# Performance work log

Measured on AMD Instinct MI355X. Metric: run time of the kernel, lower is better.

## Reference

```python
import jax, jax.numpy as jnp
import numpy as np

B, P, ENC = 64, 196, 512
EMB = ATT = DEC = 256
V = 10000
T = 44


def setup_inputs() -> dict:
    key = jax.random.key(0)
    ks = jax.random.split(key, 16)
    def xavier(k, shape):
        fan_out, fan_in = shape
        std = (2.0 / (fan_in + fan_out)) ** 0.5
        return jax.random.normal(k, shape, dtype=jnp.float32) * std
    return {
        "encoder_out": jax.random.normal(ks[0], (B, P, ENC), dtype=jnp.float32),
        "caption": jax.random.randint(ks[1], (B, T), 0, V),
        "W_enc_att": xavier(ks[2], (ATT, ENC)),
        "W_dec_att": xavier(ks[3], (ATT, DEC)),
        "W_full": xavier(ks[4], (1, ATT)),
        "embedding": jax.random.normal(ks[5], (V, EMB), dtype=jnp.float32) * 0.02,
        "W_init_h": xavier(ks[6], (DEC, ENC)),
        "b_init_h": jnp.zeros((DEC,), dtype=jnp.float32),
        "W_init_c": xavier(ks[7], (DEC, ENC)),
        "b_init_c": jnp.zeros((DEC,), dtype=jnp.float32),
        "W_ih": jax.random.normal(ks[8], (4 * DEC, EMB + ENC), dtype=jnp.float32) * 0.03,
        "b_ih": jnp.zeros((4 * DEC,), dtype=jnp.float32),
        "W_hh": jax.random.normal(ks[9], (4 * DEC, DEC), dtype=jnp.float32) * 0.03,
        "b_hh": jnp.zeros((4 * DEC,), dtype=jnp.float32),
        "W_out": xavier(ks[10], (V, DEC)),
        "b_out": jnp.zeros((V,), dtype=jnp.float32),
    }


def _decoder(encoder_out, caption, W_enc_att, W_dec_att, W_full, embedding,
             W_init_h, b_init_h, W_init_c, b_init_c,
             W_ih, b_ih, W_hh, b_hh, W_out, b_out):
    # embeddings: [B, T, EMB] -> time-major [T, B, EMB]
    emb = embedding[caption].transpose(1, 0, 2)
    # init hidden state from mean pooled encoder features
    avg = encoder_out.mean(axis=1)                      # [B, ENC]
    h0 = avg @ W_init_h.T + b_init_h                    # [B, DEC]
    c0 = avg @ W_init_c.T + b_init_c
    # attention key projection of encoder, constant over time
    att1 = jnp.einsum('bpe,ae->bpa', encoder_out, W_enc_att)  # [B, P, ATT]

    def step(carry, emb_t):
        h, c = carry
        # additive attention
        att2 = h @ W_dec_att.T                          # [B, ATT]
        scores = jnp.einsum('bpa,a->bp',
                            jax.nn.relu(att1 + att2[:, None, :]), W_full[0])
        alpha = jax.nn.softmax(scores, axis=1)          # [B, P]
        ctx = jnp.einsum('bp,bpe->be', alpha, encoder_out)  # [B, ENC]
        # LSTM cell (torch gate order: i, f, g, o)
        x = jnp.concatenate([ctx, emb_t], axis=1)       # [B, ENC+EMB]
        gates = x @ W_ih.T + b_ih + h @ W_hh.T + b_hh   # [B, 4*DEC]
        i, f, g, o = jnp.split(gates, 4, axis=1)
        c_new = jax.nn.sigmoid(f) * c + jax.nn.sigmoid(i) * jnp.tanh(g)
        h_new = jax.nn.sigmoid(o) * jnp.tanh(c_new)
        logits = h_new @ W_out.T + b_out                # [B, V]
        return (h_new, c_new), (logits, alpha)

    # NOTE: torch cat order is [weighted_context, embedding]
    (_, _), (logits, alphas) = jax.lax.scan(step, (h0, c0), emb)
    predictions = logits.transpose(1, 0, 2)             # [B, T, V]
    alphas = alphas.transpose(1, 0, 2)                  # [B, T, P]
    return predictions, alphas


def reference(encoder_out, caption, W_enc_att, W_dec_att, W_full, embedding,
              W_init_h, b_init_h, W_init_c, b_init_c,
              W_ih, b_ih, W_hh, b_hh, W_out, b_out):
    return _decoder(encoder_out, caption, W_enc_att, W_dec_att, W_full, embedding,
                    W_init_h, b_init_h, W_init_c, b_init_c,
                    W_ih, b_ih, W_hh, b_hh, W_out, b_out)
```

## Files before the change

kernel.cpp:

```cpp
#include <hip/hip_runtime.h>

#define B_   64
#define P_   196
#define ENC_ 512
#define ATT_ 256
#define DEC_ 256
#define EMB_ 256
#define V_   10000
#define T_   44
#define G4_  1024
#define XW_  768
#define A1N_ 26624

using short8 = __attribute__((ext_vector_type(8))) short;
using half8  = __attribute__((ext_vector_type(8))) _Float16;
using f32x4  = __attribute__((ext_vector_type(4))) float;
typedef _Float16 f16x2 __attribute__((ext_vector_type(2)));

__device__ __forceinline__ unsigned short f2bf(float f) {
    unsigned int u = __float_as_uint(f);
    unsigned int r = (u + 0x7fffu + ((u >> 16) & 1u)) >> 16;
    return (unsigned short)r;
}

__device__ __forceinline__ unsigned int pkh2(float a, float b) {
    f16x2 t; t.x = (_Float16)a; t.y = (_Float16)b;
    return __builtin_bit_cast(unsigned int, t);
}

__device__ __forceinline__ float fdot2f(float wbits, f16x2 xv, float acc) {
    f16x2 wv = __builtin_bit_cast(f16x2, wbits);
#if __has_builtin(__builtin_amdgcn_fdot2)
    return __builtin_amdgcn_fdot2(wv, xv, acc, false);
#else
    acc = fmaf((float)wv.x, (float)xv.x, acc);
    acc = fmaf((float)wv.y, (float)xv.y, acc);
    return acc;
#endif
}
__device__ __forceinline__ float fdot2u(unsigned int wbits, f16x2 xv, float acc) {
    f16x2 wv = __builtin_bit_cast(f16x2, wbits);
#if __has_builtin(__builtin_amdgcn_fdot2)
    return __builtin_amdgcn_fdot2(wv, xv, acc, false);
#else
    acc = fmaf((float)wv.x, (float)xv.x, acc);
    acc = fmaf((float)wv.y, (float)xv.y, acc);
    return acc;
#endif
}

__device__ __forceinline__ void bar() {
    asm volatile("s_waitcnt lgkmcnt(0)" ::: "memory");
    __builtin_amdgcn_s_barrier();
    asm volatile("" ::: "memory");
}

__global__ void k_transpose(const float* __restrict__ src, float* __restrict__ dst,
                            int N, int stride, int off) {
    __shared__ float t[32][33];
    int k0 = blockIdx.x * 32, n0 = blockIdx.y * 32;
    int tx = threadIdx.x & 31, ty = threadIdx.x >> 5;
    for (int r = ty; r < 32; r += 8)
        t[r][tx] = src[(size_t)(n0 + r) * stride + off + k0 + tx];
    __syncthreads();
    for (int r = ty; r < 32; r += 8)
        dst[(size_t)(k0 + r) * N + n0 + tx] = t[tx][r];
}

__global__ __launch_bounds__(256) void k_packWda(const float* __restrict__ Wda,
                                                 float4* __restrict__ WdaP4) {
    int d4 = blockIdx.x, a = threadIdx.x;
    float4 v;
    v.x = Wda[(size_t)a * DEC_ + 4 * d4 + 0];
    v.y = Wda[(size_t)a * DEC_ + 4 * d4 + 1];
    v.z = Wda[(size_t)a * DEC_ + 4 * d4 + 2];
    v.w = Wda[(size_t)a * DEC_ + 4 * d4 + 3];
    WdaP4[(size_t)d4 * 256 + a] = v;
}

__global__ __launch_bounds__(256) void k_packWg(const float* __restrict__ Wih,
        const float* __restrict__ Whh, float4* __restrict__ Wg4) {
    int k2 = blockIdx.x, d = threadIdx.x;
    int k = 2 * k2;
    unsigned int o[4];
#pragma unroll
    for (int g = 0; g < 4; ++g) {
        int row = g * 256 + d;
        float a0, a1;
        if (k < ENC_) {
            a0 = Wih[(size_t)row * XW_ + k];
            a1 = Wih[(size_t)row * XW_ + k + 1];
        } else {
            a0 = Whh[(size_t)row * DEC_ + k - ENC_];
            a1 = Whh[(size_t)row * DEC_ + k - ENC_ + 1];
        }
        o[g] = pkh2(a0, a1);
    }
    float4 v;
    v.x = __builtin_bit_cast(float, o[0]);
    v.y = __builtin_bit_cast(float, o[1]);
    v.z = __builtin_bit_cast(float, o[2]);
    v.w = __builtin_bit_cast(float, o[3]);
    Wg4[(size_t)k2 * 256 + d] = v;
}

__global__ __launch_bounds__(256) void k_packenc(const float* __restrict__ enc,
                                                 uint2* __restrict__ encPh) {
    int b = blockIdx.x, p4b = blockIdx.y * 7;
    for (int p4 = p4b; p4 < p4b + 7; ++p4) {
        for (int e = threadIdx.x; e < ENC_; e += 256) {
            float a0 = enc[((size_t)b * P_ + 4 * p4 + 0) * ENC_ + e];
            float a1 = enc[((size_t)b * P_ + 4 * p4 + 1) * ENC_ + e];
            float a2 = enc[((size_t)b * P_ + 4 * p4 + 2) * ENC_ + e];
            float a3 = enc[((size_t)b * P_ + 4 * p4 + 3) * ENC_ + e];
            uint2 v; v.x = pkh2(a0, a1); v.y = pkh2(a2, a3);
            encPh[((size_t)b * 49 + p4) * ENC_ + e] = v;
        }
    }
}

__global__ void k_cvt(const float* __restrict__ src, unsigned short* __restrict__ dst, int n) {
    int i = blockIdx.x * 256 + threadIdx.x;
    if (i < n) dst[i] = f2bf(src[i]);
}

__global__ __launch_bounds__(256) void k_init_state(
        const float* __restrict__ enc,
        const float* __restrict__ W_init_h, const float* __restrict__ b_init_h,
        const float* __restrict__ W_init_c, const float* __restrict__ b_init_c,
        float* __restrict__ h0, float* __restrict__ c0) {
    int b = blockIdx.x, tid = threadIdx.x;
    __shared__ float avg[ENC_];
    for (int e = tid; e < ENC_; e += 256) {
        float s = 0.f;
        const float* p = enc + (size_t)b * P_ * ENC_ + e;
        for (int i = 0; i < P_; i++) s += p[(size_t)i * ENC_];
        avg[e] = s * (1.0f / (float)P_);
    }
    __syncthreads();
    int d = tid;
    float hs = b_init_h[d], cs = b_init_c[d];
    const float* wh = W_init_h + (size_t)d * ENC_;
    const float* wc = W_init_c + (size_t)d * ENC_;
    for (int e = 0; e < ENC_; e++) { float a = avg[e]; hs += a * wh[e]; cs += a * wc[e]; }
    h0[b * DEC_ + d] = hs;
    c0[b * DEC_ + d] = cs;
}

__global__ __launch_bounds__(256) void k_att1(
        const float* __restrict__ enc, const float* __restrict__ Wea,
        unsigned int* __restrict__ att1h) {
    int n0 = blockIdx.x * 128;
    int m0 = blockIdx.y * 128;
    int b  = blockIdx.z;
    __shared__ __align__(16) unsigned short At[128][40];
    __shared__ __align__(16) unsigned short Bt[128][40];
    int tid = threadIdx.x;
    int lane = tid & 63, w = tid >> 6;
    int wm = (w & 1) * 64, wn = (w >> 1) * 64;
    f32x4 acc[4][4];
#pragma unroll
    for (int i = 0; i < 4; i++)
#pragma unroll
        for (int j = 0; j < 4; j++) acc[i][j] = (f32x4){0.f, 0.f, 0.f, 0.f};

    for (int k0 = 0; k0 < ENC_; k0 += 32) {
#pragma unroll
        for (int l = 0; l < 2; l++) {
            int idx = l * 256 + tid;
            int r = idx >> 2, kc = (idx & 3) * 8;
            const float* ap = Wea + (size_t)(m0 + r) * ENC_ + k0 + kc;
            float4 f0 = *reinterpret_cast<const float4*>(ap);
            float4 f1 = *reinterpret_cast<const float4*>(ap + 4);
            uint4 av;
            av.x = pkh2(f0.x, f0.y); av.y = pkh2(f0.z, f0.w);
            av.z = pkh2(f1.x, f1.y); av.w = pkh2(f1.z, f1.w);
            *reinterpret_cast<uint4*>(&At[r][kc]) = av;
            uint4 bv = make_uint4(0u, 0u, 0u, 0u);
            int p = n0 + r;
            if (p < P_) {
                const float* bp = enc + ((size_t)b * P_ + p) * ENC_ + k0 + kc;
                float4 g0 = *reinterpret_cast<const float4*>(bp);
                float4 g1 = *reinterpret_cast<const float4*>(bp + 4);
                bv.x = pkh2(g0.x, g0.y); bv.y = pkh2(g0.z, g0.w);
                bv.z = pkh2(g1.x, g1.y); bv.w = pkh2(g1.z, g1.w);
            }
            *reinterpret_cast<uint4*>(&Bt[r][kc]) = bv;
        }
        __syncthreads();
        int qk = (lane >> 4) * 8, fr = lane & 15;
        half8 a[4], bb[4];
#pragma unroll
        for (int i = 0; i < 4; i++) {
            a[i]  = *reinterpret_cast<const half8*>(&At[wm + i * 16 + fr][qk]);
            bb[i] = *reinterpret_cast<const half8*>(&Bt[wn + i * 16 + fr][qk]);
        }
#pragma unroll
        for (int i = 0; i < 4; i++)
#pragma unroll
            for (int j = 0; j < 4; j++)
                acc[i][j] = __builtin_amdgcn_mfma_f32_16x16x32_f16(a[i], bb[j], acc[i][j], 0, 0, 0);
        __syncthreads();
    }
    unsigned int* eb = att1h + (size_t)b * A1N_;
    int col = lane & 15, qr = (lane >> 4) * 4;
#pragma unroll
    for (int j = 0; j < 4; j++) {
        int p = n0 + wn + j * 16 + col;
        if (p < 208) {
#pragma unroll
            for (int i = 0; i < 4; i++) {
                int a0r = m0 + wm + i * 16 + qr;
                eb[(size_t)(a0r >> 1) * 208 + p]       = pkh2(acc[i][j][0], acc[i][j][1]);
                eb[(size_t)((a0r >> 1) + 1) * 208 + p] = pkh2(acc[i][j][2], acc[i][j][3]);
            }
        }
    }
}

__global__ __launch_bounds__(256) void k_embW(
        const int* __restrict__ caption, const float* __restrict__ embedding,
        const float* __restrict__ WiheT, const float* __restrict__ b_ih,
        const float* __restrict__ b_hh, float* __restrict__ embW) {
    int r0 = blockIdx.x * 16, tid = threadIdx.x;
    __shared__ float embL[16][256];
    __shared__ int capL[16];
    if (tid < 16) {
        int r = r0 + tid, t = r >> 6, b = r & 63;
        capL[tid] = caption[b * T_ + t];
    }
    __syncthreads();
#pragma unroll
    for (int lr = 0; lr < 16; lr++)
        embL[lr][tid] = embedding[(size_t)capL[lr] * EMB_ + tid];
    __syncthreads();
    float base0 = b_ih[tid] + b_hh[tid];
    float base1 = b_ih[tid + 256] + b_hh[tid + 256];
    float base2 = b_ih[tid + 512] + b_hh[tid + 512];
    float base3 = b_ih[tid + 768] + b_hh[tid + 768];
    float acc[16][4];
#pragma unroll
    for (int lr = 0; lr < 16; lr++) {
        acc[lr][0] = base0; acc[lr][1] = base1; acc[lr][2] = base2; acc[lr][3] = base3;
    }
    for (int e = 0; e < EMB_; e++) {
        const float* wr = WiheT + (size_t)e * G4_ + tid;
        float w0 = wr[0], w1 = wr[256], w2 = wr[512], w3 = wr[768];
#pragma unroll
        for (int lr = 0; lr < 16; lr++) {
            float ev = embL[lr][e];
            acc[lr][0] += w0 * ev; acc[lr][1] += w1 * ev;
            acc[lr][2] += w2 * ev; acc[lr][3] += w3 * ev;
        }
    }
#pragma unroll
    for (int lr = 0; lr < 16; lr++) {
        float* o = embW + (size_t)(r0 + lr) * G4_ + tid;
        o[0] = acc[lr][0]; o[256] = acc[lr][1]; o[512] = acc[lr][2]; o[768] = acc[lr][3];
    }
}

__global__ __launch_bounds__(1024, 4) void k_recur(
        const unsigned int* __restrict__ att1h, const float4* __restrict__ WdaP4,
        const float* __restrict__ W_full, const float4* __restrict__ Wg4,
        const float* __restrict__ embW, const uint2* __restrict__ encPh,
        const float* __restrict__ h0, const float* __restrict__ c0,
        unsigned short* __restrict__ Hbf, float* __restrict__ out_alpha) {
    int b = blockIdx.x, tid = threadIdx.x;
    int q = tid >> 8;
    int r = tid & 255;
    int e5 = tid & 511, ph = tid >> 9;

    __shared__ __align__(16) float h_l[DEC_];
    __shared__ __align__(16) float att2_l[ATT_];
    __shared__ __align__(16) float wf_l[ATT_];
    __shared__ __align__(16) _Float16 xh[XW_];
    __shared__ __align__(8)  _Float16 alpha_h[208];
    __shared__ float p1[4][256];
    __shared__ float p2[4][256];
    __shared__ float p3[2][512];
    __shared__ __align__(16) float4 p4s[4][256];
    __shared__ unsigned int att1_lds[A1N_ + 48];

    {
        const unsigned int* a1g = att1h + (size_t)b * A1N_;
        for (int i = tid; i < A1N_; i += 1024) att1_lds[i] = a1g[i];
    }
    if (tid < 256) {
        float hv = h0[b * DEC_ + tid];
        h_l[tid] = hv;
        xh[512 + tid] = (_Float16)hv;
        wf_l[tid] = W_full[tid];
    }
    float c = (tid < 256) ? c0[b * DEC_ + tid] : 0.f;
    __syncthreads();

    const uint2* encb = encPh + (size_t)b * (49 * ENC_);

    for (int t = 0; t < T_; ++t) {
        float a2 = 0.f;
#pragma unroll 4
        for (int i = 0; i < 16; i++) {
            int d4 = q * 16 + i;
            float4 w = WdaP4[(size_t)d4 * 256 + r];
            float4 h4 = *reinterpret_cast<const float4*>(&h_l[4 * d4]);
            a2 += w.x * h4.x + w.y * h4.y + w.z * h4.z + w.w * h4.w;
        }
        p1[q][r] = a2;
        bar();
        if (tid < 256) att2_l[tid] = p1[0][tid] + p1[1][tid] + p1[2][tid] + p1[3][tid];
        bar();

        float sp = 0.f;
#pragma unroll 4
        for (int i = 0; i < 32; i++) {
            int a2i = q * 32 + i;
            f16x2 av = __builtin_bit_cast(f16x2, att1_lds[a2i * 208 + r]);
            float2 t2 = *reinterpret_cast<const float2*>(&att2_l[2 * a2i]);
            float2 w4 = *reinterpret_cast<const float2*>(&wf_l[2 * a2i]);
            sp += fmaxf((float)av.x + t2.x, 0.f) * w4.x +
                  fmaxf((float)av.y + t2.y, 0.f) * w4.y;
        }
        p2[q][r] = sp;
        bar();

        float sden = 0.f;
        {
            int l = tid & 63;
#pragma unroll
            for (int cq = 0; cq < 4; cq++) {
                int cc = l + cq * 64;
                float s = p2[0][cc] + p2[1][cc] + p2[2][cc] + p2[3][cc];
                sden += (cc < P_) ? __expf(s) : 0.f;
            }
#pragma unroll
            for (int off = 32; off; off >>= 1) sden += __shfl_xor(sden, off);
        }
        if (tid < 256) {
            float s = p2[0][tid] + p2[1][tid] + p2[2][tid] + p2[3][tid];
            float ex = (tid < P_) ? __expf(s) : 0.f;
            float alpha = ex / sden;
            if (tid < 208) alpha_h[tid] = (_Float16)alpha;
            if (tid < P_) out_alpha[(size_t)b * (T_ * P_) + t * P_ + tid] = alpha;
        }
        bar();

        float cx = 0.f;
        {
            int p4b = ph ? 25 : 0, p4e = ph ? 49 : 25;
#pragma unroll 5
            for (int p4 = p4b; p4 < p4e; p4++) {
                uint2 ev = encb[(size_t)p4 * ENC_ + e5];
                f16x2 a01 = *reinterpret_cast<const f16x2*>(&alpha_h[4 * p4]);
                f16x2 a23 = *reinterpret_cast<const f16x2*>(&alpha_h[4 * p4 + 2]);
                cx = fdot2u(ev.x, a01, cx);
                cx = fdot2u(ev.y, a23, cx);
            }
        }
        p3[ph][e5] = cx;
        float ew0 = 0.f, ew1 = 0.f, ew2 = 0.f, ew3 = 0.f;
        if (tid < 256) {
            const float* ew = embW + ((size_t)t * B_ + b) * G4_;
            ew0 = ew[tid]; ew1 = ew[tid + 256]; ew2 = ew[tid + 512]; ew3 = ew[tid + 768];
        }
        bar();
        if (tid < 512) xh[tid] = (_Float16)(p3[0][tid] + p3[1][tid]);
        bar();

        float4 acc = {0.f, 0.f, 0.f, 0.f};
#pragma unroll 8
        for (int i = 0; i < 96; i++) {
            int k2 = q * 96 + i;
            float4 w = Wg4[(size_t)k2 * 256 + r];
            f16x2 xv = *reinterpret_cast<const f16x2*>(&xh[2 * k2]);
            acc.x = fdot2f(w.x, xv, acc.x);
            acc.y = fdot2f(w.y, xv, acc.y);
            acc.z = fdot2f(w.z, xv, acc.z);
            acc.w = fdot2f(w.w, xv, acc.w);
        }
        p4s[q][r] = acc;
        bar();

        if (tid < 256) {
            float4 g0 = p4s[0][tid], g1 = p4s[1][tid], g2 = p4s[2][tid], g3 = p4s[3][tid];
            float gi = g0.x + g1.x + g2.x + g3.x + ew0;
            float gf = g0.y + g1.y + g2.y + g3.y + ew1;
            float gg = g0.z + g1.z + g2.z + g3.z + ew2;
            float go = g0.w + g1.w + g2.w + g3.w + ew3;
            float i_g = 1.f / (1.f + __expf(-gi));
            float f_g = 1.f / (1.f + __expf(-gf));
            float g_g = tanhf(gg);
            float o_g = 1.f / (1.f + __expf(-go));
            c = f_g * c + i_g * g_g;
            float hn = o_g * tanhf(c);
            h_l[tid] = hn;
            xh[512 + tid] = (_Float16)hn;
            Hbf[((size_t)t * B_ + b) * DEC_ + tid] = f2bf(hn);
        }
        bar();
    }
}

__global__ __launch_bounds__(256) void k_logits(
        const unsigned short* __restrict__ Hbf, const unsigned short* __restrict__ Woutbf,
        const float* __restrict__ b_out, float* __restrict__ out) {
    int n0 = blockIdx.x * 128, m0 = blockIdx.y * 128;
    __shared__ __align__(16) unsigned short At[128][40];
    __shared__ __align__(16) unsigned short Bt[128][40];
    int tid = threadIdx.x;
    int lane = tid & 63, w = tid >> 6;
    int wm = (w & 1) * 64, wn = (w >> 1) * 64;
    f32x4 acc[4][4];
#pragma unroll
    for (int i = 0; i < 4; i++)
#pragma unroll
        for (int j = 0; j < 4; j++) acc[i][j] = (f32x4){0.f, 0.f, 0.f, 0.f};

    for (int k0 = 0; k0 < DEC_; k0 += 32) {
#pragma unroll
        for (int l = 0; l < 2; l++) {
            int idx = l * 256 + tid;
            int r = idx >> 2, kc = (idx & 3) * 8;
            uint4 av = *reinterpret_cast<const uint4*>(&Hbf[(size_t)(m0 + r) * DEC_ + k0 + kc]);
            *reinterpret_cast<uint4*>(&At[r][kc]) = av;
            uint4 bv = make_uint4(0u, 0u, 0u, 0u);
            if (n0 + r < V_)
                bv = *reinterpret_cast<const uint4*>(&Woutbf[(size_t)(n0 + r) * DEC_ + k0 + kc]);
            *reinterpret_cast<uint4*>(&Bt[r][kc]) = bv;
        }
        __syncthreads();
        int qk = (lane >> 4) * 8, fr = lane & 15;
        short8 a[4], bb[4];
#pragma unroll
        for (int i = 0; i < 4; i++) {
            a[i]  = *reinterpret_cast<const short8*>(&At[wm + i * 16 + fr][qk]);
            bb[i] = *reinterpret_cast<const short8*>(&Bt[wn + i * 16 + fr][qk]);
        }
#pragma unroll
        for (int i = 0; i < 4; i++)
#pragma unroll
            for (int j = 0; j < 4; j++)
                acc[i][j] = __builtin_amdgcn_mfma_f32_16x16x32_bf16(a[i], bb[j], acc[i][j], 0, 0, 0);
        __syncthreads();
    }
    int col = lane & 15, qr = (lane >> 4) * 4;
#pragma unroll
    for (int j = 0; j < 4; j++) {
        int n = n0 + wn + j * 16 + col;
        if (n < V_) {
            float bo = b_out[n];
#pragma unroll
            for (int i = 0; i < 4; i++)
#pragma unroll
                for (int rr = 0; rr < 4; rr++) {
                    int m = m0 + wm + i * 16 + qr + rr;
                    int t = m >> 6, bb2 = m & 63;
                    out[(size_t)bb2 * (T_ * V_) + (size_t)t * V_ + n] = acc[i][j][rr] + bo;
                }
        }
    }
}

extern "C" void kernel_launch(void* const* d_in, const int* in_sizes, int n_in,
                              void* d_out, int out_size, void* d_ws, size_t ws_size,
                              hipStream_t stream) {
    const float* enc       = (const float*)d_in[0];
    const int*   caption   = (const int*)d_in[1];
    const float* W_enc_att = (const float*)d_in[2];
    const float* W_dec_att = (const float*)d_in[3];
    const float* W_full    = (const float*)d_in[4];
    const float* embedding = (const float*)d_in[5];
    const float* W_init_h  = (const float*)d_in[6];
    const float* b_init_h  = (const float*)d_in[7];
    const float* W_init_c  = (const float*)d_in[8];
    const float* b_init_c  = (const float*)d_in[9];
    const float* W_ih      = (const float*)d_in[10];
    const float* b_ih      = (const float*)d_in[11];
    const float* W_hh      = (const float*)d_in[12];
    const float* b_hh      = (const float*)d_in[13];
    const float* W_out     = (const float*)d_in[14];
    const float* b_out     = (const float*)d_in[15];

    float* ws = (float*)d_ws;
    float* h0    = ws;
    float* c0    = ws + 16384;
    float* WdaP  = ws + 32768;
    float* WiheT = ws + 98304;
    float* Wg4   = ws + 360448;
    float* embW  = ws + 753664;
    float* att1h = ws + 3637248;
    float* encPh = ws + 5341184;
    unsigned short* Hbf    = (unsigned short*)(ws + 8552448);
    unsigned short* Woutbf = (unsigned short*)(ws + 8912896);

    float* out_pred  = (float*)d_out;
    float* out_alpha = out_pred + (size_t)B_ * T_ * V_;

    k_transpose<<<dim3(8, 32), 256, 0, stream>>>(W_ih, WiheT, G4_, XW_, ENC_);
    k_packWda<<<64, 256, 0, stream>>>(W_dec_att, (float4*)WdaP);
    k_packWg<<<384, 256, 0, stream>>>(W_ih, W_hh, (float4*)Wg4);
    k_packenc<<<dim3(64, 7), 256, 0, stream>>>(enc, (uint2*)encPh);
    k_cvt<<<10000, 256, 0, stream>>>(W_out, Woutbf, V_ * DEC_);
    k_init_state<<<B_, 256, 0, stream>>>(enc, W_init_h, b_init_h, W_init_c, b_init_c, h0, c0);
    k_att1<<<dim3(2, 2, 64), 256, 0, stream>>>(enc, W_enc_att, (unsigned int*)att1h);
    k_embW<<<176, 256, 0, stream>>>(caption, embedding, WiheT, b_ih, b_hh, embW);
    k_recur<<<B_, 1024, 0, stream>>>((const unsigned int*)att1h, (const float4*)WdaP, W_full,
                                     (const float4*)Wg4, embW, (const uint2*)encPh,
                                     h0, c0, Hbf, out_alpha);
    k_logits<<<dim3(79, 22), 256, 0, stream>>>(Hbf, Woutbf, b_out, out_pred);
}
```

Baseline: 1.309 ms.

## Split each batch row's recurrence across two cooperating blocks with flag sync

The recurrent kernel now launches two blocks per batch element. Each block redundantly computes attention, splits the context reduction unevenly, and computes half of the K dimension of the gate GEMV. Partial gate sums are exchanged through global memory using release/acquire flags and a spin-wait, halving the per-block weight streaming of the gate matrix. It relies on both blocks of a pair being co-resident and adds a cross-block handshake on every timestep.

```diff
diff --git a/kernel.cpp b/kernel.cpp
--- a/kernel.cpp
+++ b/kernel.cpp
@@ -122,6 +122,10 @@
 __global__ void k_cvt(const float* __restrict__ src, unsigned short* __restrict__ dst, int n) {
     int i = blockIdx.x * 256 + threadIdx.x;
     if (i < n) dst[i] = f2bf(src[i]);
+}
+
+__global__ void k_zeroflags(unsigned int* __restrict__ f) {
+    f[threadIdx.x] = 0u;
 }
 
 __global__ __launch_bounds__(256) void k_init_state(
@@ -265,11 +269,12 @@
         const float* __restrict__ W_full, const float4* __restrict__ Wg4,
         const float* __restrict__ embW, const uint2* __restrict__ encPh,
         const float* __restrict__ h0, const float* __restrict__ c0,
+        float* __restrict__ gpart, unsigned int* __restrict__ gflag,
         unsigned short* __restrict__ Hbf, float* __restrict__ out_alpha) {
-    int b = blockIdx.x, tid = threadIdx.x;
+    int blk = blockIdx.x, tid = threadIdx.x;
+    int pair = blk >> 1, half = blk & 1, b = pair;
     int q = tid >> 8;
     int r = tid & 255;
-    int e5 = tid & 511, ph = tid >> 9;
 
     __shared__ __align__(16) float h_l[DEC_];
     __shared__ __align__(16) float att2_l[ATT_];
@@ -298,6 +303,10 @@
     const uint2* encb = encPh + (size_t)b * (49 * ENC_);
 
     for (int t = 0; t < T_; ++t) {
+        int par = t & 1;
+        float* gme = gpart + ((size_t)blk * 2 + par) * G4_;
+        const float* gpt = gpart + ((size_t)(blk ^ 1) * 2 + par) * G4_;
+
         float a2 = 0.f;
 #pragma unroll 4
         for (int i = 0; i < 16; i++) {
@@ -341,36 +350,60 @@
             float ex = (tid < P_) ? __expf(s) : 0.f;
             float alpha = ex / sden;
             if (tid < 208) alpha_h[tid] = (_Float16)alpha;
-            if (tid < P_) out_alpha[(size_t)b * (T_ * P_) + t * P_ + tid] = alpha;
-        }
-        bar();
-
-        float cx = 0.f;
-        {
-            int p4b = ph ? 25 : 0, p4e = ph ? 49 : 25;
-#pragma unroll 5
-            for (int p4 = p4b; p4 < p4e; p4++) {
-                uint2 ev = encb[(size_t)p4 * ENC_ + e5];
-                f16x2 a01 = *reinterpret_cast<const f16x2*>(&alpha_h[4 * p4]);
-                f16x2 a23 = *reinterpret_cast<const f16x2*>(&alpha_h[4 * p4 + 2]);
-                cx = fdot2u(ev.x, a01, cx);
-                cx = fdot2u(ev.y, a23, cx);
+            if (half == 0 && tid < P_)
+                out_alpha[(size_t)b * (T_ * P_) + t * P_ + tid] = alpha;
+        }
+        bar();
+
+        if (half == 0) {
+            if (tid < 768) {
+                int php = (tid >= 384) ? 1 : 0;
+                int e2 = tid - php * 384;
+                int p4b2 = php ? 25 : 0, p4e2 = php ? 49 : 25;
+                float cx = 0.f;
+                for (int p4 = p4b2; p4 < p4e2; p4++) {
+                    uint2 ev = encb[(size_t)p4 * ENC_ + e2];
+                    f16x2 a01 = *reinterpret_cast<const f16x2*>(&alpha_h[4 * p4]);
+                    f16x2 a23 = *reinterpret_cast<const f16x2*>(&alpha_h[4 * p4 + 2]);
+                    cx = fdot2u(ev.x, a01, cx);
+                    cx = fdot2u(ev.y, a23, cx);
+                }
+                p3[php][e2] = cx;
             }
-        }
-        p3[ph][e5] = cx;
+        } else {
+            if (tid < 256) {
+                int php = tid >> 7;
+                int e2 = 384 + (tid & 127);
+                int p4b2 = php ? 25 : 0, p4e2 = php ? 49 : 25;
+                float cx = 0.f;
+                for (int p4 = p4b2; p4 < p4e2; p4++) {
+                    uint2 ev = encb[(size_t)p4 * ENC_ + e2];
+                    f16x2 a01 = *reinterpret_cast<const f16x2*>(&alpha_h[4 * p4]);
+                    f16x2 a23 = *reinterpret_cast<const f16x2*>(&alpha_h[4 * p4 + 2]);
+                    cx = fdot2u(ev.x, a01, cx);
+                    cx = fdot2u(ev.y, a23, cx);
+                }
+                p3[php][e2] = cx;
+            }
+        }
         float ew0 = 0.f, ew1 = 0.f, ew2 = 0.f, ew3 = 0.f;
         if (tid < 256) {
             const float* ew = embW + ((size_t)t * B_ + b) * G4_;
             ew0 = ew[tid]; ew1 = ew[tid + 256]; ew2 = ew[tid + 512]; ew3 = ew[tid + 768];
         }
         bar();
-        if (tid < 512) xh[tid] = (_Float16)(p3[0][tid] + p3[1][tid]);
+        if (half == 0) {
+            if (tid < 384) xh[tid] = (_Float16)(p3[0][tid] + p3[1][tid]);
+        } else {
+            if (tid < 128) xh[384 + tid] = (_Float16)(p3[0][384 + tid] + p3[1][384 + tid]);
+        }
         bar();
 
         float4 acc = {0.f, 0.f, 0.f, 0.f};
+        int kb = half * 192 + q * 48;
 #pragma unroll 8
-        for (int i = 0; i < 96; i++) {
-            int k2 = q * 96 + i;
+        for (int i = 0; i < 48; i++) {
+            int k2 = kb + i;
             float4 w = Wg4[(size_t)k2 * 256 + r];
             f16x2 xv = *reinterpret_cast<const f16x2*>(&xh[2 * k2]);
             acc.x = fdot2f(w.x, xv, acc.x);
@@ -379,14 +412,39 @@
             acc.w = fdot2f(w.w, xv, acc.w);
         }
         p4s[q][r] = acc;
-        bar();
-
+        __syncthreads();
+
+        float4 own = {0.f, 0.f, 0.f, 0.f};
         if (tid < 256) {
             float4 g0 = p4s[0][tid], g1 = p4s[1][tid], g2 = p4s[2][tid], g3 = p4s[3][tid];
-            float gi = g0.x + g1.x + g2.x + g3.x + ew0;
-            float gf = g0.y + g1.y + g2.y + g3.y + ew1;
-            float gg = g0.z + g1.z + g2.z + g3.z + ew2;
-            float go = g0.w + g1.w + g2.w + g3.w + ew3;
+            own.x = g0.x + g1.x + g2.x + g3.x;
+            own.y = g0.y + g1.y + g2.y + g3.y;
+            own.z = g0.z + g1.z + g2.z + g3.z;
+            own.w = g0.w + g1.w + g2.w + g3.w;
+            __hip_atomic_store(&gme[tid],       own.x, __ATOMIC_RELAXED, __HIP_MEMORY_SCOPE_AGENT);
+            __hip_atomic_store(&gme[tid + 256], own.y, __ATOMIC_RELAXED, __HIP_MEMORY_SCOPE_AGENT);
+            __hip_atomic_store(&gme[tid + 512], own.z, __ATOMIC_RELAXED, __HIP_MEMORY_SCOPE_AGENT);
+            __hip_atomic_store(&gme[tid + 768], own.w, __ATOMIC_RELAXED, __HIP_MEMORY_SCOPE_AGENT);
+        }
+        __syncthreads();
+        if (tid == 0) {
+            __hip_atomic_store(&gflag[blk], (unsigned int)(t + 1),
+                               __ATOMIC_RELEASE, __HIP_MEMORY_SCOPE_AGENT);
+            while (__hip_atomic_load(&gflag[blk ^ 1], __ATOMIC_ACQUIRE,
+                                     __HIP_MEMORY_SCOPE_AGENT) < (unsigned int)(t + 1))
+                __builtin_amdgcn_s_sleep(2);
+        }
+        __syncthreads();
+
+        if (tid < 256) {
+            float px = __hip_atomic_load(&gpt[tid],       __ATOMIC_RELAXED, __HIP_MEMORY_SCOPE_AGENT);
+            float py = __hip_atomic_load(&gpt[tid + 256], __ATOMIC_RELAXED, __HIP_MEMORY_SCOPE_AGENT);
+            float pz = __hip_atomic_load(&gpt[tid + 512], __ATOMIC_RELAXED, __HIP_MEMORY_SCOPE_AGENT);
+            float pw = __hip_atomic_load(&gpt[tid + 768], __ATOMIC_RELAXED, __HIP_MEMORY_SCOPE_AGENT);
+            float gi = (own.x + px) + ew0;
+            float gf = (own.y + py) + ew1;
+            float gg = (own.z + pz) + ew2;
+            float go = (own.w + pw) + ew3;
             float i_g = 1.f / (1.f + __expf(-gi));
             float f_g = 1.f / (1.f + __expf(-gf));
             float g_g = tanhf(gg);
@@ -395,7 +453,8 @@
             float hn = o_g * tanhf(c);
             h_l[tid] = hn;
             xh[512 + tid] = (_Float16)hn;
-            Hbf[((size_t)t * B_ + b) * DEC_ + tid] = f2bf(hn);
+            if (half == 0)
+                Hbf[((size_t)t * B_ + b) * DEC_ + tid] = f2bf(hn);
         }
         bar();
     }
@@ -492,6 +551,8 @@
     float* encPh = ws + 5341184;
     unsigned short* Hbf    = (unsigned short*)(ws + 8552448);
     unsigned short* Woutbf = (unsigned short*)(ws + 8912896);
+    float* gpart = ws + 10192896;
+    unsigned int* gflag = (unsigned int*)(ws + 10455040);
 
     float* out_pred  = (float*)d_out;
     float* out_alpha = out_pred + (size_t)B_ * T_ * V_;
@@ -501,11 +562,12 @@
     k_packWg<<<384, 256, 0, stream>>>(W_ih, W_hh, (float4*)Wg4);
     k_packenc<<<dim3(64, 7), 256, 0, stream>>>(enc, (uint2*)encPh);
     k_cvt<<<10000, 256, 0, stream>>>(W_out, Woutbf, V_ * DEC_);
+    k_zeroflags<<<1, 128, 0, stream>>>(gflag);
     k_init_state<<<B_, 256, 0, stream>>>(enc, W_init_h, b_init_h, W_init_c, b_init_c, h0, c0);
     k_att1<<<dim3(2, 2, 64), 256, 0, stream>>>(enc, W_enc_att, (unsigned int*)att1h);
     k_embW<<<176, 256, 0, stream>>>(caption, embedding, WiheT, b_ih, b_hh, embW);
-    k_recur<<<B_, 1024, 0, stream>>>((const unsigned int*)att1h, (const float4*)WdaP, W_full,
-                                     (const float4*)Wg4, embW, (const uint2*)encPh,
-                                     h0, c0, Hbf, out_alpha);
+    k_recur<<<128, 1024, 0, stream>>>((const unsigned int*)att1h, (const float4*)WdaP, W_full,
+                                      (const float4*)Wg4, embW, (const uint2*)encPh,
+                                      h0, c0, gpart, gflag, Hbf, out_alpha);
     k_logits<<<dim3(79, 22), 256, 0, stream>>>(Hbf, Woutbf, b_out, out_pred);
 }
```

New measurement: 1.176 ms. 10.2% less time.
